# Performance work log

Measured on AMD Instinct MI355X. Metric: run time of the kernel, lower is better.

## Reference

```python
import jax, jax.numpy as jnp
import numpy as np

D = 512  # common_dim

def _ln(x, g, b):
    m = jnp.mean(x, -1, keepdims=True)
    v = jnp.var(x, -1, keepdims=True)
    return g * (x - m) * jax.lax.rsqrt(v + 1e-5) + b

def _gelu(x):
    return jax.nn.gelu(x, approximate=False)  # torch nn.GELU default (erf)

def _mha(q, kv, Wi, bi, Wo, bo):
    # seq_len == 1: softmax over a single key is exactly 1 regardless of q/k,
    # so MultiheadAttention reduces to out_proj(v_proj(kv)); identical math,
    # and q/k projections receive exactly zero gradient either way.
    vp = kv @ Wi[:, 2 * D:] + bi[2 * D:]
    return vp @ Wo + bo

def setup_inputs() -> dict:
    key = jax.random.key(0)
    ks = iter(jax.random.split(key, 64))
    B, HID = 8192, 1024
    Fv, Fi, Ft = 10, 6, 15
    def rn(shape, s=0.02):
        return jax.random.normal(next(ks), shape, jnp.float32) * s
    return dict(
        verb_hidden=rn((B, HID), 1.0), verb_logits=rn((B, Fv), 1.0),
        inst_hidden=rn((B, HID), 1.0), inst_logits=rn((B, Fi), 1.0),
        target_hidden=rn((B, HID), 1.0), target_logits=rn((B, Ft), 1.0),
        # hidden_projection per task (order: verb, instrument, target)
        hp_W=rn((3, HID, D)), hp_b=jnp.zeros((3, D)), hp_g=jnp.ones((3, D)), hp_be=jnp.zeros((3, D)),
        # logit_projection per task (different in-dims)
        lp_W_verb=rn((Fv, D // 2)), lp_b_verb=jnp.zeros((D // 2,)),
        lp_W_inst=rn((Fi, D // 2)), lp_b_inst=jnp.zeros((D // 2,)),
        lp_W_target=rn((Ft, D // 2)), lp_b_target=jnp.zeros((D // 2,)),
        lp_g=jnp.ones((3, D // 2)), lp_be=jnp.zeros((3, D // 2)),
        # 4 MHA modules: [self, verb_inst, verb_target, inst_target]
        mha_in_W=rn((4, D, 3 * D)), mha_in_b=jnp.zeros((4, 3 * D)),
        mha_out_W=rn((4, D, D)), mha_out_b=jnp.zeros((4, D)),
        n1_g=jnp.ones((3, D)), n1_be=jnp.zeros((3, D)),
        n2_g=jnp.ones((3, D)), n2_be=jnp.zeros((3, D)),
        gate_W=rn((3, 2 * D, D)), gate_b=jnp.zeros((3, D)),
        fus_W1=rn((3 * D + 3 * (D // 2), D)), fus_b1=jnp.zeros((D,)),
        fus_g1=jnp.ones((D,)), fus_ge1=jnp.zeros((D,)),
        fus_W2=rn((D, D)), fus_b2=jnp.zeros((D,)),
        fus_g2=jnp.ones((D,)), fus_ge2=jnp.zeros((D,)),
    )

def reference(verb_hidden, verb_logits, inst_hidden, inst_logits, target_hidden, target_logits,
              hp_W, hp_b, hp_g, hp_be,
              lp_W_verb, lp_b_verb, lp_W_inst, lp_b_inst, lp_W_target, lp_b_target, lp_g, lp_be,
              mha_in_W, mha_in_b, mha_out_W, mha_out_b,
              n1_g, n1_be, n2_g, n2_be, gate_W, gate_b,
              fus_W1, fus_b1, fus_g1, fus_ge1, fus_W2, fus_b2, fus_g2, fus_ge2):
    # dropout is inference-mode identity
    def hproj(x, i):
        return _gelu(_ln(x @ hp_W[i] + hp_b[i], hp_g[i], hp_be[i]))
    def lproj(x, W, b, i):
        return _gelu(_ln(jax.nn.sigmoid(x) @ W + b, lp_g[i], lp_be[i]))

    verb_h, inst_h, target_h = hproj(verb_hidden, 0), hproj(inst_hidden, 1), hproj(target_hidden, 2)
    verb_l = lproj(verb_logits, lp_W_verb, lp_b_verb, 0)
    inst_l = lproj(inst_logits, lp_W_inst, lp_b_inst, 1)
    target_l = lproj(target_logits, lp_W_target, lp_b_target, 2)

    sa = lambda x: _mha(x, x, mha_in_W[0], mha_in_b[0], mha_out_W[0], mha_out_b[0])
    verb_e = _ln(verb_h + sa(verb_h), n1_g[0], n1_be[0])
    inst_e = _ln(inst_h + sa(inst_h), n1_g[1], n1_be[1])
    target_e = _ln(target_h + sa(target_h), n1_g[2], n1_be[2])

    ca = lambda i, q, kv: _mha(q, kv, mha_in_W[i], mha_in_b[i], mha_out_W[i], mha_out_b[i])
    v2i, i2v = ca(1, verb_e, inst_e), ca(1, inst_e, verb_e)
    v2t, t2v = ca(2, verb_e, target_e), ca(2, target_e, verb_e)
    i2t, t2i = ca(3, inst_e, target_e), ca(3, target_e, inst_e)

    def fuse(x, a, b, i):
        m = (a + b) * 0.5
        gate = jax.nn.sigmoid(jnp.concatenate([x, m], axis=1) @ gate_W[i] + gate_b[i])
        return _ln(x + gate * m, n2_g[i], n2_be[i])

    verb_f = fuse(verb_e, v2i, v2t, 0)
    inst_f = fuse(inst_e, i2v, i2t, 1)
    target_f = fuse(target_e, t2v, t2i, 2)

    comb = jnp.concatenate([verb_f, inst_f, target_f, verb_l, inst_l, target_l], axis=1)  # [B, 2304]
    h = _gelu(_ln(comb @ fus_W1 + fus_b1, fus_g1, fus_ge1))
    return _ln(h @ fus_W2 + fus_b2, fus_g2, fus_ge2)
```

## Files before the change

kernel.cpp:

```cpp
#include <hip/hip_runtime.h>
#include <math.h>

typedef unsigned short ushort_t;
using short8  = __attribute__((ext_vector_type(8))) short;
using floatx4 = __attribute__((ext_vector_type(4))) float;

__device__ __forceinline__ ushort_t f2bf(float f) {
  unsigned u = __builtin_bit_cast(unsigned, f);
  u = (u + 0x7fffu + ((u >> 16) & 1u)) >> 16;
  return (ushort_t)u;
}
__device__ __forceinline__ float bf2f(ushort_t u) {
  unsigned v = ((unsigned)u) << 16;
  return __builtin_bit_cast(float, v);
}

__device__ __forceinline__ void load_lds16(const ushort_t* g, ushort_t* l) {
  __builtin_amdgcn_global_load_lds(
      (const __attribute__((address_space(1))) unsigned int*)g,
      (__attribute__((address_space(3))) unsigned int*)l, 16, 0, 0);
}

struct Seg { const ushort_t* A; const ushort_t* W; int lda, ldw, K; };
struct GemmZ {
  ushort_t* Cb;
  ushort_t* CbT;
  const float* bias;
  float scale; int nseg; int mmax;
  Seg seg[6];
};
struct GemmArgs { GemmZ z[9]; };

template <int BM, int TAG>
__global__ __launch_bounds__(256) void gemm_bt(GemmArgs ga) {
  const GemmZ& gz = ga.z[blockIdx.z];
  if ((int)blockIdx.x >= gz.mmax) return;
  __shared__ ushort_t As[BM * 32];
  __shared__ ushort_t Bs[128 * 32];
  const int tid = threadIdx.x;
  const int wid = tid >> 6, lane = tid & 63, quad = lane >> 4, l16 = lane & 15;
  const int bm = blockIdx.x * BM, bn = blockIdx.y * 128;
  constexpr int MI = BM / 32;
  const int wm = (wid & 1) * (BM / 2), wn = (wid >> 1) * 64;
  floatx4 acc[MI][4] = {};
  const int srow = tid >> 2, scol = (tid & 3) * 8;
  ushort_t* aL = As + tid * 8;
  ushort_t* bL = Bs + tid * 8;

  for (int s = 0; s < gz.nseg; s++) {
    const Seg sg = gz.seg[s];
    const ushort_t* aG = sg.A + (size_t)(bm + srow) * sg.lda + scol;
    const ushort_t* bG = sg.W + (size_t)(bn + srow) * sg.ldw + scol;
    const size_t astep = (size_t)64 * sg.lda;
    const size_t bstep = (size_t)64 * sg.ldw;
    for (int k0 = 0; k0 < sg.K; k0 += 32) {
      __syncthreads();
      load_lds16(aG + k0, aL);
      if (BM == 128) load_lds16(aG + k0 + astep, aL + 2048);
      load_lds16(bG + k0, bL);
      load_lds16(bG + k0 + bstep, bL + 2048);
      __syncthreads();
      short8 af[MI], bf[4];
#pragma unroll
      for (int i = 0; i < MI; i++)
        af[i] = *(const short8*)&As[(wm + 16 * i + l16) * 32 + quad * 8];
#pragma unroll
      for (int j = 0; j < 4; j++)
        bf[j] = *(const short8*)&Bs[(wn + 16 * j + l16) * 32 + quad * 8];
#pragma unroll
      for (int i = 0; i < MI; i++)
#pragma unroll
        for (int j = 0; j < 4; j++)
          acc[i][j] = __builtin_amdgcn_mfma_f32_16x16x32_bf16(af[i], bf[j], acc[i][j], 0, 0, 0);
    }
  }

#pragma unroll
  for (int i = 0; i < MI; i++) {
#pragma unroll
    for (int j = 0; j < 4; j++) {
      const int colg = bn + wn + 16 * j + l16;
      const float bb = gz.bias ? gz.bias[colg] : 0.f;
#pragma unroll
      for (int r = 0; r < 4; r++) {
        const int rowg = bm + wm + 16 * i + quad * 4 + r;
        const float v = (acc[i][j][r] + bb) * gz.scale;
        const ushort_t bo = f2bf(v);
        if (gz.Cb)  gz.Cb[(size_t)rowg * 512 + colg] = bo;
        if (gz.CbT) gz.CbT[(size_t)colg * 512 + rowg] = bo;
      }
    }
  }
}

__global__ __launch_bounds__(256) void row_ln(
    const ushort_t* __restrict__ P, const ushort_t* __restrict__ R,
    const ushort_t* __restrict__ cross,
    const float* __restrict__ gamma, const float* __restrict__ beta, int gstride,
    ushort_t* __restrict__ outb, float* __restrict__ outf, int mode, int gelu)
{
  const size_t S2 = (size_t)8192 * 512;
  const int wid = threadIdx.x >> 6, lane = threadIdx.x & 63;
  const int row = blockIdx.x * 4 + wid;
  const int t = row >> 13;
  const float* g  = gamma + t * gstride;
  const float* be = beta + t * gstride;
  const ushort_t* p = P + (size_t)row * 512;
  const ushort_t* ar = nullptr;
  if (mode == 2) ar = cross + (size_t)t * S2 + (size_t)(row & 8191) * 512;
  float v[8], s = 0.f, ss = 0.f;
#pragma unroll
  for (int j = 0; j < 8; j++) {
    const int c = lane + j * 64;
    float x = bf2f(p[c]);
    if (mode == 2) {
      const float sg = 1.f / (1.f + __expf(-x));
      x = bf2f(R[(size_t)row * 512 + c]) + sg * bf2f(ar[c]);
    } else if (mode == 1) {
      x += bf2f(R[(size_t)row * 512 + c]);
    }
    v[j] = x; s += x; ss += x * x;
  }
#pragma unroll
  for (int off = 32; off > 0; off >>= 1) {
    s  += __shfl_xor(s,  off, 64);
    ss += __shfl_xor(ss, off, 64);
  }
  const float mean = s * (1.f / 512.f);
  const float var  = ss * (1.f / 512.f) - mean * mean;
  const float rstd = rsqrtf(var + 1e-5f);
#pragma unroll
  for (int j = 0; j < 8; j++) {
    const int c = lane + j * 64;
    float y = g[c] * ((v[j] - mean) * rstd) + be[c];
    if (gelu) y = 0.5f * y * (1.f + erff(y * 0.70710678118f));
    if (outb) outb[(size_t)row * 512 + c] = f2bf(y);
    else      outf[(size_t)row * 512 + c] = y;
  }
}

__global__ __launch_bounds__(256) void lproj3(
    const float* __restrict__ vl, const float* __restrict__ il, const float* __restrict__ tl,
    const float* __restrict__ Wv, const float* __restrict__ bv,
    const float* __restrict__ Wi, const float* __restrict__ bi,
    const float* __restrict__ Wt, const float* __restrict__ bt,
    const float* __restrict__ lp_g, const float* __restrict__ lp_be,
    ushort_t* __restrict__ out)
{
  const int set = blockIdx.y;
  const float* logits = set == 0 ? vl : set == 1 ? il : tl;
  const int F = set == 0 ? 10 : set == 1 ? 6 : 15;
  const float* W    = set == 0 ? Wv : set == 1 ? Wi : Wt;
  const float* bias = set == 0 ? bv : set == 1 ? bi : bt;
  const float* gamma = lp_g + set * 256;
  const float* beta  = lp_be + set * 256;
  ushort_t* o = out + (size_t)set * 8192 * 256;
  const int wid = threadIdx.x >> 6, lane = threadIdx.x & 63;
  const int row = blockIdx.x * 4 + wid;
  float sg[16];
  for (int f = 0; f < F; f++)
    sg[f] = 1.f / (1.f + __expf(-logits[(size_t)row * F + f]));
  float v[4], s = 0.f, ss = 0.f;
#pragma unroll
  for (int j = 0; j < 4; j++) {
    const int c = lane + j * 64;
    float a = bias[c];
    for (int f = 0; f < F; f++) a += sg[f] * W[f * 256 + c];
    v[j] = a; s += a; ss += a * a;
  }
#pragma unroll
  for (int off = 32; off > 0; off >>= 1) {
    s  += __shfl_xor(s,  off, 64);
    ss += __shfl_xor(ss, off, 64);
  }
  const float mean = s * (1.f / 256.f);
  const float var  = ss * (1.f / 256.f) - mean * mean;
  const float rstd = rsqrtf(var + 1e-5f);
#pragma unroll
  for (int j = 0; j < 4; j++) {
    const int c = lane + j * 64;
    float y = gamma[c] * ((v[j] - mean) * rstd) + beta[c];
    y = 0.5f * y * (1.f + erff(y * 0.70710678118f));
    o[(size_t)row * 256 + c] = f2bf(y);
  }
}

struct PrepArgs {
  const float *vh, *ih, *th;
  const float *mha_in_W, *mha_out_W, *mha_in_b, *mha_out_b;
  const float *hp_W, *gate_W, *fus_W1, *fus_W2;
  ushort_t *xbf, *Wvbf, *hpWt, *gateWt, *fusW1t, *fusW2t, *WoT;
  float *cb;
};

__global__ __launch_bounds__(256) void prep(PrepArgs pa) {
  __shared__ float tsh[32][33];
  const int b = blockIdx.x, tid = threadIdx.x;
  if (b < 24576) {
    const int mat = b >> 13, blk = b & 8191;
    const float* src = mat == 0 ? pa.vh : mat == 1 ? pa.ih : pa.th;
    const size_t i = (size_t)blk * 256 + tid;
    const float4 f = ((const float4*)src)[i];
    ushort4 o; o.x = f2bf(f.x); o.y = f2bf(f.y); o.z = f2bf(f.z); o.w = f2bf(f.w);
    ((ushort4*)(pa.xbf + (size_t)mat * 8192 * 1024))[i] = o;
    return;
  }
  if (b < 28672) {
    const int u = b - 24576, z = u >> 10, blk = u & 1023;
    const int idx = blk * 256 + tid, r = idx >> 9, c = idx & 511;
    pa.Wvbf[(size_t)z * 262144 + idx] =
        f2bf(pa.mha_in_W[(size_t)z * 786432 + (size_t)r * 1536 + 1024 + c]);
    return;
  }
  if (b >= 34176) {
    const int u2 = b - 34176, z = u2 >> 1, part = u2 & 1;
    const int n = part * 256 + tid;
    const float* bv = pa.mha_in_b + z * 1536 + 1024;
    const float* Wo = pa.mha_out_W + (size_t)z * 262144;
    float a = pa.mha_out_b[z * 512 + n];
    for (int k = 0; k < 512; k++) a += bv[k] * Wo[(size_t)k * 512 + n];
    pa.cb[z * 512 + n] = a;
    return;
  }
  const float* tin; ushort_t* tout; int K, N, u; size_t izs, ozs;
  if (b < 30208)      { u = b - 28672; tin = pa.hp_W;      tout = pa.hpWt;   K = 1024; N = 512; izs = 524288; ozs = 524288; }
  else if (b < 31744) { u = b - 30208; tin = pa.gate_W;    tout = pa.gateWt; K = 1024; N = 512; izs = 524288; ozs = 524288; }
  else if (b < 32896) { u = b - 31744; tin = pa.fus_W1;    tout = pa.fusW1t; K = 2304; N = 512; izs = 0;      ozs = 0; }
  else if (b < 33152) { u = b - 32896; tin = pa.fus_W2;    tout = pa.fusW2t; K = 512;  N = 512; izs = 0;      ozs = 0; }
  else                { u = b - 33152; tin = pa.mha_out_W; tout = pa.WoT;    K = 512;  N = 512; izs = 262144; ozs = 262144; }
  const int nbx = N / 32, perz = nbx * (K / 32);
  const int z = u / perz, rem = u % perz, bx = rem % nbx, by = rem / nbx;
  tin += (size_t)z * izs; tout += (size_t)z * ozs;
  const int n0 = bx * 32, k0 = by * 32;
  const int tx = tid & 31, ty = tid >> 5;
#pragma unroll
  for (int r = 0; r < 32; r += 8)
    tsh[ty + r][tx] = tin[(size_t)(k0 + ty + r) * N + n0 + tx];
  __syncthreads();
#pragma unroll
  for (int r = 0; r < 32; r += 8)
    tout[(size_t)(n0 + ty + r) * K + k0 + tx] = f2bf(tsh[tx][ty + r]);
}

__global__ __launch_bounds__(256) void bias2_k(
    const float* __restrict__ cb, const float* __restrict__ gate_W,
    const float* __restrict__ gate_b, float* __restrict__ out,
    float* __restrict__ out2)
{
  const int t = blockIdx.z;
  const int m1[3] = {1, 1, 2}, m2[3] = {2, 3, 3};
  const float* c1 = cb + m1[t] * 512;
  const float* c2 = cb + m2[t] * 512;
  const float* W = gate_W + (size_t)t * 524288 + (size_t)512 * 512;
  const int n = blockIdx.x * 256 + threadIdx.x;
  float a = gate_b[t * 512 + n];
  for (int k = 0; k < 512; k++) a += 0.5f * (c1[k] + c2[k]) * W[(size_t)k * 512 + n];
  out[t * 512 + n] = a;
  out2[t * 512 + n] = c1[n] + c2[n];
}

extern "C" void kernel_launch(void* const* d_in, const int* in_sizes, int n_in,
                              void* d_out, int out_size, void* d_ws, size_t ws_size,
                              hipStream_t stream)
{
  const float* verb_hidden   = (const float*)d_in[0];
  const float* verb_logits   = (const float*)d_in[1];
  const float* inst_hidden   = (const float*)d_in[2];
  const float* inst_logits   = (const float*)d_in[3];
  const float* target_hidden = (const float*)d_in[4];
  const float* target_logits = (const float*)d_in[5];
  const float* hp_W  = (const float*)d_in[6];
  const float* hp_b  = (const float*)d_in[7];
  const float* hp_g  = (const float*)d_in[8];
  const float* hp_be = (const float*)d_in[9];
  const float* lp_W_verb   = (const float*)d_in[10];
  const float* lp_b_verb   = (const float*)d_in[11];
  const float* lp_W_inst   = (const float*)d_in[12];
  const float* lp_b_inst   = (const float*)d_in[13];
  const float* lp_W_target = (const float*)d_in[14];
  const float* lp_b_target = (const float*)d_in[15];
  const float* lp_g  = (const float*)d_in[16];
  const float* lp_be = (const float*)d_in[17];
  const float* mha_in_W  = (const float*)d_in[18];
  const float* mha_in_b  = (const float*)d_in[19];
  const float* mha_out_W = (const float*)d_in[20];
  const float* mha_out_b = (const float*)d_in[21];
  const float* n1_g  = (const float*)d_in[22];
  const float* n1_be = (const float*)d_in[23];
  const float* n2_g  = (const float*)d_in[24];
  const float* n2_be = (const float*)d_in[25];
  const float* gate_W = (const float*)d_in[26];
  const float* gate_b = (const float*)d_in[27];
  const float* fus_W1 = (const float*)d_in[28];
  const float* fus_b1 = (const float*)d_in[29];
  const float* fus_g1 = (const float*)d_in[30];
  const float* fus_ge1= (const float*)d_in[31];
  const float* fus_W2 = (const float*)d_in[32];
  const float* fus_b2 = (const float*)d_in[33];
  const float* fus_g2 = (const float*)d_in[34];
  const float* fus_ge2= (const float*)d_in[35];

  char* w = (char*)d_ws;
  const size_t S2 = (size_t)8192 * 512;
  const size_t MB = 1024 * 1024;
  ushort_t* xbf     = (ushort_t*)(w);
  ushort_t* crossbf = (ushort_t*)(w);
  ushort_t* gbf     = (ushort_t*)(w);
  ushort_t* Pbig    = (ushort_t*)(w + 48 * MB);
  ushort_t* hbf     = (ushort_t*)(w + 72 * MB);
  ushort_t* fbf     = (ushort_t*)(w + 72 * MB);
  ushort_t* ebf     = (ushort_t*)(w + 96 * MB);
  ushort_t* lbf     = (ushort_t*)(w + 120 * MB);
  char* wp = w + 132 * MB;
  ushort_t* hpWt    = (ushort_t*)(wp);
  ushort_t* gateWt  = (ushort_t*)(wp + 3145728);
  ushort_t* fusW1t  = (ushort_t*)(wp + 6291456);
  ushort_t* fusW2t  = (ushort_t*)(wp + 8650752);
  ushort_t* WoT     = (ushort_t*)(wp + 9175040);
  ushort_t* Wvbf    = (ushort_t*)(wp + 11272192);
  ushort_t* CWt     = (ushort_t*)(wp + 13369344);
  ushort_t* CWplain = (ushort_t*)(wp + 15466496);
  ushort_t* Gt      = (ushort_t*)(wp + 17563648);
  float*    cb      = (float*)(wp + 20709376);
  float*    bias2   = (float*)(wp + 20717568);
  float*    cbsum   = (float*)(wp + 20723712);

  dim3 blk(256);
  const int mods[3][2] = {{1, 2}, {1, 3}, {2, 3}};
  const int srcs[3][2] = {{1, 2}, {0, 2}, {0, 1}};

  {
    PrepArgs pa;
    pa.vh = verb_hidden; pa.ih = inst_hidden; pa.th = target_hidden;
    pa.mha_in_W = mha_in_W; pa.mha_out_W = mha_out_W;
    pa.mha_in_b = mha_in_b; pa.mha_out_b = mha_out_b;
    pa.hp_W = hp_W; pa.gate_W = gate_W; pa.fus_W1 = fus_W1; pa.fus_W2 = fus_W2;
    pa.xbf = xbf; pa.Wvbf = Wvbf; pa.hpWt = hpWt; pa.gateWt = gateWt;
    pa.fusW1t = fusW1t; pa.fusW2t = fusW2t; pa.WoT = WoT; pa.cb = cb;
    prep<<<34184, blk, 0, stream>>>(pa);
  }

  {
    GemmArgs ga{};
    for (int z = 0; z < 4; z++) {
      GemmZ& g = ga.z[z];
      g.Cb = CWplain + (size_t)z * 262144; g.CbT = CWt + (size_t)z * 262144;
      g.scale = 1.f; g.nseg = 1; g.mmax = 4;
      g.seg[0] = {Wvbf + (size_t)z * 262144, WoT + (size_t)z * 262144, 512, 512, 512};
    }
    gemm_bt<128, 2><<<dim3(4, 4, 4), blk, 0, stream>>>(ga);
  }

  bias2_k<<<dim3(2, 1, 3), blk, 0, stream>>>(cb, gate_W, gate_b, bias2, cbsum);

  {
    GemmArgs ga{};
    for (int z = 0; z < 3; z++) {
      GemmZ& g = ga.z[z];
      g.Cb = Pbig + (size_t)z * S2; g.bias = hp_b + z * 512;
      g.scale = 1.f; g.nseg = 1; g.mmax = 64;
      g.seg[0] = {xbf + (size_t)z * 8192 * 1024, hpWt + (size_t)z * 524288, 1024, 1024, 1024};
    }
    for (int idx = 0; idx < 6; idx++) {
      const int t = idx >> 1, u = idx & 1, m = mods[t][u];
      GemmZ& g = ga.z[3 + idx];
      g.Cb = Gt + (size_t)idx * 262144; g.scale = 0.5f; g.nseg = 1; g.mmax = 4;
      g.seg[0] = {gateWt + (size_t)t * 524288 + 512, CWplain + (size_t)m * 262144, 1024, 512, 512};
    }
    gemm_bt<128, 4><<<dim3(64, 4, 9), blk, 0, stream>>>(ga);
  }

  lproj3<<<dim3(2048, 3), blk, 0, stream>>>(verb_logits, inst_logits, target_logits,
      lp_W_verb, lp_b_verb, lp_W_inst, lp_b_inst, lp_W_target, lp_b_target,
      lp_g, lp_be, lbf);

  row_ln<<<6144, blk, 0, stream>>>(Pbig, nullptr, nullptr, hp_g, hp_be, 512,
                                   hbf, nullptr, 0, 1);

  {
    GemmArgs ga{};
    GemmZ& g = ga.z[0];
    g.Cb = Pbig; g.bias = cb; g.scale = 1.f; g.nseg = 1; g.mmax = 192;
    g.seg[0] = {hbf, CWt, 512, 512, 512};
    gemm_bt<128, 7><<<dim3(192, 4, 1), blk, 0, stream>>>(ga);
  }
  row_ln<<<6144, blk, 0, stream>>>(Pbig, hbf, nullptr, n1_g, n1_be, 512,
                                   ebf, nullptr, 1, 0);

  {
    GemmArgs ga{};
    for (int t = 0; t < 3; t++) {
      GemmZ& g = ga.z[t];
      g.Cb = crossbf + (size_t)t * S2;
      g.bias = cbsum + t * 512; g.scale = 0.5f; g.nseg = 2; g.mmax = 64;
      g.seg[0] = {ebf + (size_t)srcs[t][0] * S2, CWt + (size_t)mods[t][0] * 262144, 512, 512, 512};
      g.seg[1] = {ebf + (size_t)srcs[t][1] * S2, CWt + (size_t)mods[t][1] * 262144, 512, 512, 512};
    }
    for (int t = 0; t < 3; t++) {
      GemmZ& g = ga.z[3 + t];
      g.Cb = Pbig + (size_t)t * S2; g.bias = bias2 + t * 512;
      g.scale = 1.f; g.nseg = 3; g.mmax = 64;
      g.seg[0] = {ebf + (size_t)t * S2,           gateWt + (size_t)t * 524288, 512, 1024, 512};
      g.seg[1] = {ebf + (size_t)srcs[t][0] * S2,  Gt + (size_t)(2 * t) * 262144,     512, 512, 512};
      g.seg[2] = {ebf + (size_t)srcs[t][1] * S2,  Gt + (size_t)(2 * t + 1) * 262144, 512, 512, 512};
    }
    gemm_bt<128, 9><<<dim3(64, 4, 6), blk, 0, stream>>>(ga);
  }

  row_ln<<<6144, blk, 0, stream>>>(Pbig, ebf, crossbf, n2_g, n2_be, 512,
                                   fbf, nullptr, 2, 0);

  {
    GemmArgs ga{};
    GemmZ& g = ga.z[0];
    g.Cb = Pbig; g.bias = fus_b1; g.scale = 1.f; g.nseg = 6; g.mmax = 128;
    g.seg[0] = {fbf,                          fusW1t,        512, 2304, 512};
    g.seg[1] = {fbf + S2,                     fusW1t + 512,  512, 2304, 512};
    g.seg[2] = {fbf + 2 * S2,                 fusW1t + 1024, 512, 2304, 512};
    g.seg[3] = {lbf,                          fusW1t + 1536, 256, 2304, 256};
    g.seg[4] = {lbf + (size_t)8192 * 256,     fusW1t + 1792, 256, 2304, 256};
    g.seg[5] = {lbf + (size_t)2 * 8192 * 256, fusW1t + 2048, 256, 2304, 256};
    gemm_bt<64, 11><<<dim3(128, 4, 1), blk, 0, stream>>>(ga);
  }
  row_ln<<<2048, blk, 0, stream>>>(Pbig, nullptr, nullptr, fus_g1, fus_ge1, 0,
                                   gbf, nullptr, 0, 1);
  {
    GemmArgs ga{};
    GemmZ& g = ga.z[0];
    g.Cb = Pbig; g.bias = fus_b2; g.scale = 1.f; g.nseg = 1; g.mmax = 128;
    g.seg[0] = {gbf, fusW2t, 512, 512, 512};
    gemm_bt<64, 13><<<dim3(128, 4, 1), blk, 0, stream>>>(ga);
  }
  row_ln<<<2048, blk, 0, stream>>>(Pbig, nullptr, nullptr, fus_g2, fus_ge2, 0,
                                   nullptr, (float*)d_out, 0, 0);
}
```

Baseline: 658.4 us.

## Double-buffer LDS tiles in the bf16 GEMM to overlap loads with MFMA

The GEMM's shared-memory A/B tiles become two ping-pong buffers. The next K-tile, possibly from the next segment, is issued with global_load_lds while MFMAs run on the current tile. The K loop across segments is flattened into one tile counter, which drops to one barrier per iteration. This hides global-to-LDS latency at the cost of twice the LDS per block, which may reduce occupancy.

```diff
diff --git a/kernel.cpp b/kernel.cpp
--- a/kernel.cpp
+++ b/kernel.cpp
@@ -35,8 +35,8 @@
 __global__ __launch_bounds__(256) void gemm_bt(GemmArgs ga) {
   const GemmZ& gz = ga.z[blockIdx.z];
   if ((int)blockIdx.x >= gz.mmax) return;
-  __shared__ ushort_t As[BM * 32];
-  __shared__ ushort_t Bs[128 * 32];
+  __shared__ ushort_t As[2][BM * 32];
+  __shared__ ushort_t Bs[2][128 * 32];
   const int tid = threadIdx.x;
   const int wid = tid >> 6, lane = tid & 63, quad = lane >> 4, l16 = lane & 15;
   const int bm = blockIdx.x * BM, bn = blockIdx.y * 128;
@@ -44,35 +44,52 @@
   const int wm = (wid & 1) * (BM / 2), wn = (wid >> 1) * 64;
   floatx4 acc[MI][4] = {};
   const int srow = tid >> 2, scol = (tid & 3) * 8;
-  ushort_t* aL = As + tid * 8;
-  ushort_t* bL = Bs + tid * 8;
-
-  for (int s = 0; s < gz.nseg; s++) {
-    const Seg sg = gz.seg[s];
-    const ushort_t* aG = sg.A + (size_t)(bm + srow) * sg.lda + scol;
-    const ushort_t* bG = sg.W + (size_t)(bn + srow) * sg.ldw + scol;
-    const size_t astep = (size_t)64 * sg.lda;
-    const size_t bstep = (size_t)64 * sg.ldw;
-    for (int k0 = 0; k0 < sg.K; k0 += 32) {
-      __syncthreads();
-      load_lds16(aG + k0, aL);
-      if (BM == 128) load_lds16(aG + k0 + astep, aL + 2048);
-      load_lds16(bG + k0, bL);
-      load_lds16(bG + k0 + bstep, bL + 2048);
-      __syncthreads();
-      short8 af[MI], bf[4];
-#pragma unroll
-      for (int i = 0; i < MI; i++)
-        af[i] = *(const short8*)&As[(wm + 16 * i + l16) * 32 + quad * 8];
+
+  int nt = 0;
+  for (int s = 0; s < gz.nseg; s++) nt += gz.seg[s].K >> 5;
+
+  int ss = 0, ks = 0, KC = 0;
+  const ushort_t *aC = nullptr, *bC = nullptr;
+  size_t aStep = 0, bStep = 0;
+  auto setseg = [&]() {
+    const Seg& sg = gz.seg[ss];
+    aC = sg.A + (size_t)(bm + srow) * sg.lda + scol;
+    bC = sg.W + (size_t)(bn + srow) * sg.ldw + scol;
+    aStep = (size_t)64 * sg.lda;
+    bStep = (size_t)64 * sg.ldw;
+    KC = sg.K;
+  };
+  auto stage = [&](int buf) {
+    ushort_t* aL = &As[buf][tid * 8];
+    ushort_t* bL = &Bs[buf][tid * 8];
+    load_lds16(aC + ks, aL);
+    if constexpr (BM == 128) load_lds16(aC + ks + aStep, aL + 2048);
+    load_lds16(bC + ks, bL);
+    load_lds16(bC + ks + bStep, bL + 2048);
+    ks += 32;
+    if (ks >= KC) { ks = 0; if (++ss < gz.nseg) setseg(); }
+  };
+
+  setseg();
+  stage(0);
+  __syncthreads();
+  int cur = 0;
+  for (int t = 0; t < nt; t++) {
+    if (t + 1 < nt) stage(cur ^ 1);
+    short8 af[MI], bw[4];
+#pragma unroll
+    for (int i = 0; i < MI; i++)
+      af[i] = *(const short8*)&As[cur][(wm + 16 * i + l16) * 32 + quad * 8];
+#pragma unroll
+    for (int j = 0; j < 4; j++)
+      bw[j] = *(const short8*)&Bs[cur][(wn + 16 * j + l16) * 32 + quad * 8];
+#pragma unroll
+    for (int i = 0; i < MI; i++)
 #pragma unroll
       for (int j = 0; j < 4; j++)
-        bf[j] = *(const short8*)&Bs[(wn + 16 * j + l16) * 32 + quad * 8];
-#pragma unroll
-      for (int i = 0; i < MI; i++)
-#pragma unroll
-        for (int j = 0; j < 4; j++)
-          acc[i][j] = __builtin_amdgcn_mfma_f32_16x16x32_bf16(af[i], bf[j], acc[i][j], 0, 0, 0);
-    }
+        acc[i][j] = __builtin_amdgcn_mfma_f32_16x16x32_bf16(af[i], bw[j], acc[i][j], 0, 0, 0);
+    __syncthreads();
+    cur ^= 1;
   }
 
 #pragma unroll
```

Result: no change. 659.8 us (+0.2%).

## Double GEMM K-tile to 64 with XOR-swizzled LDS layout

Applied to the files above, without the earlier changes.

The GEMM K step grows from 32 to 64, which halves the number of barrier pairs per K loop. Each thread now loads 16-byte chunks into an XOR-swizzled LDS layout (column chunk XORed with row mod 8) to avoid bank conflicts on the wider rows. The fragment reads use the same swizzle, and two MFMAs are issued per A/B pair. LDS use doubles, which may reduce occupancy, and segments with K=256 still divide evenly by 64. The template tags are replaced by separately named kernel wrappers.

```diff
diff --git a/kernel.cpp b/kernel.cpp
--- a/kernel.cpp
+++ b/kernel.cpp
@@ -31,47 +31,52 @@
 };
 struct GemmArgs { GemmZ z[9]; };
 
-template <int BM, int TAG>
-__global__ __launch_bounds__(256) void gemm_bt(GemmArgs ga) {
+template <int BM>
+__device__ __forceinline__ void gemm_body(const GemmArgs& ga) {
   const GemmZ& gz = ga.z[blockIdx.z];
   if ((int)blockIdx.x >= gz.mmax) return;
-  __shared__ ushort_t As[BM * 32];
-  __shared__ ushort_t Bs[128 * 32];
+  __shared__ ushort_t As[BM * 64];
+  __shared__ ushort_t Bs[128 * 64];
   const int tid = threadIdx.x;
   const int wid = tid >> 6, lane = tid & 63, quad = lane >> 4, l16 = lane & 15;
   const int bm = blockIdx.x * BM, bn = blockIdx.y * 128;
   constexpr int MI = BM / 32;
   const int wm = (wid & 1) * (BM / 2), wn = (wid >> 1) * 64;
   floatx4 acc[MI][4] = {};
-  const int srow = tid >> 2, scol = (tid & 3) * 8;
-  ushort_t* aL = As + tid * 8;
-  ushort_t* bL = Bs + tid * 8;
+  const int srow = tid >> 3;
+  const int scol = ((tid & 7) ^ (srow & 7)) << 3;
+  const int x7 = l16 & 7;
 
   for (int s = 0; s < gz.nseg; s++) {
     const Seg sg = gz.seg[s];
     const ushort_t* aG = sg.A + (size_t)(bm + srow) * sg.lda + scol;
     const ushort_t* bG = sg.W + (size_t)(bn + srow) * sg.ldw + scol;
-    const size_t astep = (size_t)64 * sg.lda;
-    const size_t bstep = (size_t)64 * sg.ldw;
-    for (int k0 = 0; k0 < sg.K; k0 += 32) {
+    for (int k0 = 0; k0 < sg.K; k0 += 64) {
       __syncthreads();
-      load_lds16(aG + k0, aL);
-      if (BM == 128) load_lds16(aG + k0 + astep, aL + 2048);
-      load_lds16(bG + k0, bL);
-      load_lds16(bG + k0 + bstep, bL + 2048);
+#pragma unroll
+      for (int r = 0; r < BM / 32; r++)
+        load_lds16(aG + k0 + (size_t)(32 * r) * sg.lda, As + r * 2048 + tid * 8);
+#pragma unroll
+      for (int r = 0; r < 4; r++)
+        load_lds16(bG + k0 + (size_t)(32 * r) * sg.ldw, Bs + r * 2048 + tid * 8);
       __syncthreads();
-      short8 af[MI], bf[4];
-#pragma unroll
-      for (int i = 0; i < MI; i++)
-        af[i] = *(const short8*)&As[(wm + 16 * i + l16) * 32 + quad * 8];
+      short8 bw[4][2];
 #pragma unroll
       for (int j = 0; j < 4; j++)
-        bf[j] = *(const short8*)&Bs[(wn + 16 * j + l16) * 32 + quad * 8];
-#pragma unroll
-      for (int i = 0; i < MI; i++)
-#pragma unroll
-        for (int j = 0; j < 4; j++)
-          acc[i][j] = __builtin_amdgcn_mfma_f32_16x16x32_bf16(af[i], bf[j], acc[i][j], 0, 0, 0);
+#pragma unroll
+        for (int h = 0; h < 2; h++)
+          bw[j][h] = *(const short8*)&Bs[(wn + 16 * j + l16) * 64 + (((quad + 4 * h) ^ x7) << 3)];
+#pragma unroll
+      for (int i = 0; i < MI; i++) {
+        const int rb = (wm + 16 * i + l16) * 64;
+        short8 a0 = *(const short8*)&As[rb + ((quad ^ x7) << 3)];
+        short8 a1 = *(const short8*)&As[rb + (((quad + 4) ^ x7) << 3)];
+#pragma unroll
+        for (int j = 0; j < 4; j++) {
+          acc[i][j] = __builtin_amdgcn_mfma_f32_16x16x32_bf16(a0, bw[j][0], acc[i][j], 0, 0, 0);
+          acc[i][j] = __builtin_amdgcn_mfma_f32_16x16x32_bf16(a1, bw[j][1], acc[i][j], 0, 0, 0);
+        }
+      }
     }
   }
 
@@ -92,6 +97,13 @@
     }
   }
 }
+
+__global__ __launch_bounds__(256) void gemm_L2(GemmArgs ga)  { gemm_body<128>(ga); }
+__global__ __launch_bounds__(256) void gemm_L4(GemmArgs ga)  { gemm_body<128>(ga); }
+__global__ __launch_bounds__(256) void gemm_L7(GemmArgs ga)  { gemm_body<128>(ga); }
+__global__ __launch_bounds__(256) void gemm_L9(GemmArgs ga)  { gemm_body<128>(ga); }
+__global__ __launch_bounds__(256) void gemm_L11(GemmArgs ga) { gemm_body<64>(ga); }
+__global__ __launch_bounds__(256) void gemm_L13(GemmArgs ga) { gemm_body<64>(ga); }
 
 __global__ __launch_bounds__(256) void row_ln(
     const ushort_t* __restrict__ P, const ushort_t* __restrict__ R,
@@ -348,7 +360,7 @@
       g.scale = 1.f; g.nseg = 1; g.mmax = 4;
       g.seg[0] = {Wvbf + (size_t)z * 262144, WoT + (size_t)z * 262144, 512, 512, 512};
     }
-    gemm_bt<128, 2><<<dim3(4, 4, 4), blk, 0, stream>>>(ga);
+    gemm_L2<<<dim3(4, 4, 4), blk, 0, stream>>>(ga);
   }
 
   bias2_k<<<dim3(2, 1, 3), blk, 0, stream>>>(cb, gate_W, gate_b, bias2, cbsum);
@@ -367,7 +379,7 @@
       g.Cb = Gt + (size_t)idx * 262144; g.scale = 0.5f; g.nseg = 1; g.mmax = 4;
       g.seg[0] = {gateWt + (size_t)t * 524288 + 512, CWplain + (size_t)m * 262144, 1024, 512, 512};
     }
-    gemm_bt<128, 4><<<dim3(64, 4, 9), blk, 0, stream>>>(ga);
+    gemm_L4<<<dim3(64, 4, 9), blk, 0, stream>>>(ga);
   }
 
   lproj3<<<dim3(2048, 3), blk, 0, stream>>>(verb_logits, inst_logits, target_logits,
@@ -382,7 +394,7 @@
     GemmZ& g = ga.z[0];
     g.Cb = Pbig; g.bias = cb; g.scale = 1.f; g.nseg = 1; g.mmax = 192;
     g.seg[0] = {hbf, CWt, 512, 512, 512};
-    gemm_bt<128, 7><<<dim3(192, 4, 1), blk, 0, stream>>>(ga);
+    gemm_L7<<<dim3(192, 4, 1), blk, 0, stream>>>(ga);
   }
   row_ln<<<6144, blk, 0, stream>>>(Pbig, hbf, nullptr, n1_g, n1_be, 512,
                                    ebf, nullptr, 1, 0);
@@ -404,7 +416,7 @@
       g.seg[1] = {ebf + (size_t)srcs[t][0] * S2,  Gt + (size_t)(2 * t) * 262144,     512, 512, 512};
       g.seg[2] = {ebf + (size_t)srcs[t][1] * S2,  Gt + (size_t)(2 * t + 1) * 262144, 512, 512, 512};
     }
-    gemm_bt<128, 9><<<dim3(64, 4, 6), blk, 0, stream>>>(ga);
+    gemm_L9<<<dim3(64, 4, 6), blk, 0, stream>>>(ga);
   }
 
   row_ln<<<6144, blk, 0, stream>>>(Pbig, ebf, crossbf, n2_g, n2_be, 512,
@@ -420,7 +432,7 @@
     g.seg[3] = {lbf,                          fusW1t + 1536, 256, 2304, 256};
     g.seg[4] = {lbf + (size_t)8192 * 256,     fusW1t + 1792, 256, 2304, 256};
     g.seg[5] = {lbf + (size_t)2 * 8192 * 256, fusW1t + 2048, 256, 2304, 256};
-    gemm_bt<64, 11><<<dim3(128, 4, 1), blk, 0, stream>>>(ga);
+    gemm_L11<<<dim3(128, 4, 1), blk, 0, stream>>>(ga);
   }
   row_ln<<<2048, blk, 0, stream>>>(Pbig, nullptr, nullptr, fus_g1, fus_ge1, 0,
                                    gbf, nullptr, 0, 1);
@@ -429,7 +441,7 @@
     GemmZ& g = ga.z[0];
     g.Cb = Pbig; g.bias = fus_b2; g.scale = 1.f; g.nseg = 1; g.mmax = 128;
     g.seg[0] = {gbf, fusW2t, 512, 512, 512};
-    gemm_bt<64, 13><<<dim3(128, 4, 1), blk, 0, stream>>>(ga);
+    gemm_L13<<<dim3(128, 4, 1), blk, 0, stream>>>(ga);
   }
   row_ln<<<2048, blk, 0, stream>>>(Pbig, nullptr, nullptr, fus_g2, fus_ge2, 0,
                                    nullptr, (float*)d_out, 0, 0);
```

Measured after the change: 633.9 us. 3.7% less time.
